# Kernel optimization log

Measured on AMD Instinct MI355X. Metric: run time of the kernel, lower is better.

Reference implementation:

```python
import jax, jax.numpy as jnp
import numpy as np

B, N, DIM, H = 8, 4096, 768, 12
HD = DIM // H
SCALE = HD ** -0.5


def setup_inputs() -> dict:
    key = jax.random.key(0)
    ks = jax.random.split(key, 6)
    x = jax.random.normal(ks[0], (B, N, DIM), dtype=jnp.float32)
    # torch nn.Linear weights: [out_features, in_features]
    Wqkv = jax.random.normal(ks[1], (3 * DIM, DIM), dtype=jnp.float32) * (DIM ** -0.5)
    Wp = jax.random.normal(ks[2], (DIM, DIM), dtype=jnp.float32) * (DIM ** -0.5)
    bp = jnp.zeros((DIM,), dtype=jnp.float32)
    w_q = jax.random.normal(ks[3], (H, HD), dtype=jnp.float32)
    w_k = jax.random.normal(ks[4], (H, HD), dtype=jnp.float32)
    return {"x": x, "Wqkv": Wqkv, "Wp": Wp, "bp": bp, "w_q": w_q, "w_k": w_k}


def reference(x, Wqkv, Wp, bp, w_q, w_k):
    b, n, c = x.shape
    qkv = x @ Wqkv.T                                   # [B,N,3C]
    # rearrange 'B N (qkv H C) -> qkv B H N C'
    qkv = qkv.reshape(b, n, 3, H, HD).transpose(2, 0, 3, 1, 4)
    q, k, v = qkv[0], qkv[1], qkv[2]                   # each [B,H,N,hd]

    alpha = jnp.einsum('bhnc,hc->bhn', q, w_q) * SCALE
    alpha = jax.nn.softmax(alpha, axis=-1)             # [B,H,N]
    global_q = jnp.einsum('bhn,bhnc->bhc', alpha, q)   # [B,H,hd]

    p = global_q[:, :, None, :] * k                    # [B,H,N,hd]
    beta = jnp.einsum('bhnc,hc->bhn', p, w_k) * SCALE
    beta = jax.nn.softmax(beta, axis=-1)
    global_k = jnp.einsum('bhn,bhnc->bhc', beta, k)    # [B,H,hd]

    u = global_k[:, :, None, :] * v                    # [B,H,N,hd]
    q_flat = q.transpose(0, 2, 1, 3).reshape(b, n, c)  # 'B H N C -> B N (H C)'
    u_flat = u.transpose(0, 2, 1, 3).reshape(b, n, c)
    return u_flat @ Wp.T + bp + q_flat
```

## Files before the change

### kernel.cpp

```cpp
#include <hip/hip_runtime.h>
#include <hip/hip_bf16.h>
#include <cstdint>
#include <cstddef>

#define B_ 8
#define N_ 4096
#define DIM_ 768
#define H_ 12
#define M_ (B_*N_)
#define SCALE_ 0.125f
#define NS2 16
#define KDIM 768
#define NKT 12
#define NITER 6

typedef __attribute__((ext_vector_type(8))) short s8v;
typedef __attribute__((ext_vector_type(4))) float f4v;

__device__ inline float bf2f(unsigned short u) {
    unsigned v = ((unsigned)u) << 16;
    return __builtin_bit_cast(float, v);
}
__device__ inline unsigned short f2bf(float f) {
    unsigned u = __builtin_bit_cast(unsigned, f);
    return (unsigned short)((u + 0x7FFFu + ((u >> 16) & 1u)) >> 16);
}
__device__ inline void gload16(const void* g, void* l) {
    __builtin_amdgcn_global_load_lds(
        (const __attribute__((address_space(1))) void*)g,
        (__attribute__((address_space(3))) void*)l, 16, 0, 0);
}

#define BARX() __builtin_amdgcn_s_barrier()
#define PRIO1() __builtin_amdgcn_s_setprio(1)
#define PRIO0() __builtin_amdgcn_s_setprio(0)
#define VM4() asm volatile("s_waitcnt vmcnt(4)" ::: "memory")
#define VM0() asm volatile("s_waitcnt vmcnt(0)" ::: "memory")

__global__ __launch_bounds__(512, 2)
void gemm8(const unsigned short* __restrict__ A, int ldaE,
           const unsigned short* __restrict__ Bmat,
           unsigned short* __restrict__ Cb,
           const float* __restrict__ w_q,
           float* __restrict__ pv1, float* __restrict__ pms1,
           int ntn)
{
    __shared__ __align__(16) char smem[131072];
    const int tid = threadIdx.x;
    const int l = tid & 63, w = tid >> 6;
    const int lr = l & 15, g = l >> 4;
    const int wm = w >> 2, wn = w & 3;

    const int nwg = gridDim.x, cpx = nwg >> 3;
    const int bid = blockIdx.x;
    const int lg = (bid & 7) * cpx + (bid >> 3);
    const int tm = lg / ntn, tn = lg % ntn;
    const int m0 = tm * 256, n0 = tn * 256;

    const long ldaB = (long)ldaE * 2;
    const long ldbB = (long)KDIM * 2;

    const int srA = w * 8 + (l >> 3);
    const int kbs = (l & 7) * 16;
    const int kbx = kbs ^ ((srA & 7) << 4);
    long offA[2], offB[2];
    offA[0] = (long)(srA) * ldaB + kbx;
    offA[1] = (long)(128 + srA) * ldaB + kbx;
    offB[0] = (long)(((srA >> 5)) * 64 + (srA & 31)) * ldbB + kbx;
    offB[1] = (long)((2 + (srA >> 5)) * 64 + (srA & 31)) * ldbB + kbx;

    const char* Abase = (const char*)(A + (size_t)m0 * ldaE);
    const char* Bbase = (const char*)(Bmat + (size_t)n0 * KDIM);

    const int aoff = (wm * 64 + lr) * 128;
    const int boff = (wn * 32 + lr) * 128;
    const int kx0 = (g * 16) ^ ((lr & 7) << 4);
    const int kx1 = (64 + g * 16) ^ ((lr & 7) << 4);

    f4v acc[8][4] = {};
    s8v af[4][2];
    s8v bfr[2][2][2];

#define STG_A(buf_, qm_, kt_) { \
    const char* s0_ = Abase + (long)(kt_) * 2 + (long)(qm_) * 64 * ldaB; \
    char* d0_ = smem + ((buf_) * 4 + (qm_)) * 16384 + w * 1024; \
    gload16(s0_ + offA[0], d0_); \
    gload16(s0_ + offA[1], d0_ + 8192); }

#define STG_B(buf_, qn_, kt_) { \
    const char* s0_ = Bbase + (long)(kt_) * 2 + (long)(qn_) * 32 * ldbB; \
    char* d0_ = smem + ((buf_) * 4 + 2 + (qn_)) * 16384 + w * 1024; \
    gload16(s0_ + offB[0], d0_); \
    gload16(s0_ + offB[1], d0_ + 8192); }

#define DS_A(buf_, qm_) { \
    const char* ba_ = smem + ((buf_) * 4 + (qm_)) * 16384 + aoff; \
    af[0][0] = *(const s8v*)(ba_ +    0 + kx0); af[0][1] = *(const s8v*)(ba_ +    0 + kx1); \
    af[1][0] = *(const s8v*)(ba_ + 2048 + kx0); af[1][1] = *(const s8v*)(ba_ + 2048 + kx1); \
    af[2][0] = *(const s8v*)(ba_ + 4096 + kx0); af[2][1] = *(const s8v*)(ba_ + 4096 + kx1); \
    af[3][0] = *(const s8v*)(ba_ + 6144 + kx0); af[3][1] = *(const s8v*)(ba_ + 6144 + kx1); }

#define DS_B(buf_, qn_) { \
    const char* bb_ = smem + ((buf_) * 4 + 2 + (qn_)) * 16384 + boff; \
    bfr[qn_][0][0] = *(const s8v*)(bb_ +    0 + kx0); bfr[qn_][0][1] = *(const s8v*)(bb_ +    0 + kx1); \
    bfr[qn_][1][0] = *(const s8v*)(bb_ + 2048 + kx0); bfr[qn_][1][1] = *(const s8v*)(bb_ + 2048 + kx1); }

#define MM(fmg_, fng_, qn_, kk_) \
    acc[fmg_][fng_] = __builtin_amdgcn_mfma_f32_16x16x32_bf16(af[(fmg_)&3][kk_], bfr[qn_][(fng_)&1][kk_], acc[fmg_][fng_], 0, 0, 0);

#define MFMA8(qm_, qn_, kk_) \
    MM((qm_)*4+0, (qn_)*2+0, qn_, kk_) MM((qm_)*4+0, (qn_)*2+1, qn_, kk_) \
    MM((qm_)*4+1, (qn_)*2+0, qn_, kk_) MM((qm_)*4+1, (qn_)*2+1, qn_, kk_) \
    MM((qm_)*4+2, (qn_)*2+0, qn_, kk_) MM((qm_)*4+2, (qn_)*2+1, qn_, kk_) \
    MM((qm_)*4+3, (qn_)*2+0, qn_, kk_) MM((qm_)*4+3, (qn_)*2+1, qn_, kk_)

#define MFMA16(qm_, qn_) { MFMA8(qm_, qn_, 0) MFMA8(qm_, qn_, 1) }

    STG_A(0, 0, 0); STG_B(0, 0, 0); STG_A(0, 1, 0); STG_B(0, 1, 0);
    STG_A(1, 0, 64); STG_B(1, 0, 64);
    VM4(); BARX();

    for (int i = 0; i < NITER; ++i) {
        const int t1k = (2 * i + 1) * 64, t2k = (2 * i + 2) * 64, t3k = (2 * i + 3) * 64;
        const bool h2 = (2 * i + 2) < NKT, h3 = (2 * i + 3) < NKT;
        const bool last = (i == NITER - 1);
        DS_A(0, 0); DS_B(0, 0); STG_B(1, 1, t1k);
        BARX(); PRIO1(); MFMA16(0, 0); PRIO0(); BARX();
        DS_B(0, 1); STG_A(1, 1, t1k);
        BARX(); PRIO1(); MFMA16(0, 1); PRIO0(); BARX();
        DS_A(0, 1); if (h2) STG_A(0, 0, t2k);
        BARX(); PRIO1(); MFMA16(1, 0); PRIO0(); BARX();
        if (h2) STG_B(0, 0, t2k);
        BARX(); PRIO1(); MFMA16(1, 1); PRIO0();
        if (last) { VM0(); } else { VM4(); }
        BARX();
        DS_A(1, 0); DS_B(1, 0); if (h2) STG_A(0, 1, t2k);
        BARX(); PRIO1(); MFMA16(0, 0); PRIO0(); BARX();
        DS_B(1, 1); if (h2) STG_B(0, 1, t2k);
        BARX(); PRIO1(); MFMA16(0, 1); PRIO0(); BARX();
        DS_A(1, 1); if (h3) STG_A(1, 0, t3k);
        BARX(); PRIO1(); MFMA16(1, 0); PRIO0(); BARX();
        if (h3) STG_B(1, 0, t3k);
        BARX(); PRIO1(); MFMA16(1, 1); PRIO0();
        if (last) { VM0(); } else { VM4(); }
        BARX();
    }

    if (tn >= 3) {
        const int c0 = (tn - 3) * 256;
#pragma unroll
        for (int fmg = 0; fmg < 8; ++fmg) {
#pragma unroll
            for (int fng = 0; fng < 4; ++fng) {
                const int col = c0 + wn * 64 + fng * 16 + lr;
#pragma unroll
                for (int r = 0; r < 4; ++r) {
                    const int row = m0 + wm * 128 + fmg * 16 + g * 4 + r;
                    Cb[(size_t)row * DIM_ + col] = f2bf(acc[fmg][fng][r]);
                }
            }
        }
    }

    if (tn < 3) {
        const int h = tn * 4 + wn;
        float wq[4];
#pragma unroll
        for (int f = 0; f < 4; ++f) wq[f] = w_q[h * 64 + f * 16 + lr];

        float d[8][4];
#pragma unroll
        for (int fmg = 0; fmg < 8; ++fmg) {
#pragma unroll
            for (int r = 0; r < 4; ++r) {
                float s = acc[fmg][0][r] * wq[0] + acc[fmg][1][r] * wq[1]
                        + acc[fmg][2][r] * wq[2] + acc[fmg][3][r] * wq[3];
                s += __shfl_xor(s, 1); s += __shfl_xor(s, 2);
                s += __shfl_xor(s, 4); s += __shfl_xor(s, 8);
                d[fmg][r] = s * SCALE_;
            }
        }
        float mw = d[0][0];
#pragma unroll
        for (int fmg = 0; fmg < 8; ++fmg)
#pragma unroll
            for (int r = 0; r < 4; ++r) mw = fmaxf(mw, d[fmg][r]);
        mw = fmaxf(mw, __shfl_xor(mw, 16));
        mw = fmaxf(mw, __shfl_xor(mw, 32));

        float ssum = 0.f;
        float pvec[4] = {};
#pragma unroll
        for (int fmg = 0; fmg < 8; ++fmg) {
#pragma unroll
            for (int r = 0; r < 4; ++r) {
                const float e = __expf(d[fmg][r] - mw);
                ssum += e;
#pragma unroll
                for (int f = 0; f < 4; ++f) pvec[f] += e * acc[fmg][f][r];
            }
        }
        ssum += __shfl_xor(ssum, 16); ssum += __shfl_xor(ssum, 32);
#pragma unroll
        for (int f = 0; f < 4; ++f) {
            pvec[f] += __shfl_xor(pvec[f], 16);
            pvec[f] += __shfl_xor(pvec[f], 32);
        }

        const int b = m0 >> 12;
        const int bh = b * H_ + h;
        const int slice = ((m0 & (N_ - 1)) >> 7) + wm;
        if (g == 0) {
#pragma unroll
            for (int f = 0; f < 4; ++f)
                pv1[(size_t)(bh * 32 + slice) * 64 + f * 16 + lr] = pvec[f];
            if (lr == 0) {
                pms1[(bh * 32 + slice) * 2] = mw;
                pms1[(bh * 32 + slice) * 2 + 1] = ssum;
            }
        }
    }
#undef STG_A
#undef STG_B
#undef DS_A
#undef DS_B
#undef MM
#undef MFMA8
#undef MFMA16
}

template<int MODE>
__global__ __launch_bounds__(512, 2)
void gemm128(const unsigned short* __restrict__ A, int ldaE,
             const unsigned short* __restrict__ Bmat,
             float* __restrict__ Cf, unsigned short* __restrict__ CbO,
             const float* __restrict__ bias, const float* __restrict__ addW,
             int Nc, int ntn)
{
    __shared__ __align__(16) char smem[98304];
    const int tid = threadIdx.x;
    const int l = tid & 63, w = tid >> 6;
    const int lr = l & 15, g = l >> 4;
    const int wm = w >> 2, wn = w & 3;

    const int nwg = gridDim.x, cpx = nwg >> 3;
    const int bid = blockIdx.x;
    const int lg = (bid & 7) * cpx + (bid >> 3);
    const int tm = lg / ntn, tn = lg % ntn;
    const int m0 = tm * 128, n0 = tn * 256;

    const long ldaB = (long)ldaE * 2;
    const long ldbB = (long)KDIM * 2;

    const unsigned short* Bp = Bmat;
    if (MODE == 0) Bp = Bmat + (size_t)(m0 >> 12) * (DIM_ * DIM_);

    const int srA = w * 8 + (l >> 3);
    const int kbs = (l & 7) * 16;
    const int kbx = kbs ^ ((srA & 7) << 4);
    long offA[2], offB[2];
    offA[0] = (long)(srA) * ldaB + kbx;
    offA[1] = (long)(64 + srA) * ldaB + kbx;
    offB[0] = (long)(((srA >> 5)) * 64 + (srA & 31)) * ldbB + kbx;
    offB[1] = (long)((2 + (srA >> 5)) * 64 + (srA & 31)) * ldbB + kbx;

    const char* Abase = (const char*)(A + (size_t)m0 * ldaE);
    const char* Bbase = (const char*)(Bp + (size_t)n0 * KDIM);

    const int aoff = (wm * 64 + lr) * 128;
    const int boff = (wn * 32 + lr) * 128;
    const int kx0 = (g * 16) ^ ((lr & 7) << 4);
    const int kx1 = (64 + g * 16) ^ ((lr & 7) << 4);

    f4v acc[4][4] = {};
    s8v af[4][2];
    s8v bfr[2][2][2];

#define STG_A1(buf_, kt_) { \
    const char* s0_ = Abase + (long)(kt_) * 2; \
    char* d0_ = smem + ((buf_) * 3) * 16384 + w * 1024; \
    gload16(s0_ + offA[0], d0_); \
    gload16(s0_ + offA[1], d0_ + 8192); }

#define STG_B1(buf_, qn_, kt_) { \
    const char* s0_ = Bbase + (long)(kt_) * 2 + (long)(qn_) * 32 * ldbB; \
    char* d0_ = smem + ((buf_) * 3 + 1 + (qn_)) * 16384 + w * 1024; \
    gload16(s0_ + offB[0], d0_); \
    gload16(s0_ + offB[1], d0_ + 8192); }

#define DS_A1(buf_) { \
    const char* ba_ = smem + ((buf_) * 3) * 16384 + aoff; \
    af[0][0] = *(const s8v*)(ba_ +    0 + kx0); af[0][1] = *(const s8v*)(ba_ +    0 + kx1); \
    af[1][0] = *(const s8v*)(ba_ + 2048 + kx0); af[1][1] = *(const s8v*)(ba_ + 2048 + kx1); \
    af[2][0] = *(const s8v*)(ba_ + 4096 + kx0); af[2][1] = *(const s8v*)(ba_ + 4096 + kx1); \
    af[3][0] = *(const s8v*)(ba_ + 6144 + kx0); af[3][1] = *(const s8v*)(ba_ + 6144 + kx1); }

#define DS_B1(buf_, qn_) { \
    const char* bb_ = smem + ((buf_) * 3 + 1 + (qn_)) * 16384 + boff; \
    bfr[qn_][0][0] = *(const s8v*)(bb_ +    0 + kx0); bfr[qn_][0][1] = *(const s8v*)(bb_ +    0 + kx1); \
    bfr[qn_][1][0] = *(const s8v*)(bb_ + 2048 + kx0); bfr[qn_][1][1] = *(const s8v*)(bb_ + 2048 + kx1); }

#define MM1(fm_, fng_, qn_, kk_) \
    acc[fm_][fng_] = __builtin_amdgcn_mfma_f32_16x16x32_bf16(af[fm_][kk_], bfr[qn_][(fng_)&1][kk_], acc[fm_][fng_], 0, 0, 0);

#define MFMA16_1(qn_, kk_) \
    MM1(0, (qn_)*2+0, qn_, kk_) MM1(0, (qn_)*2+1, qn_, kk_) \
    MM1(1, (qn_)*2+0, qn_, kk_) MM1(1, (qn_)*2+1, qn_, kk_) \
    MM1(2, (qn_)*2+0, qn_, kk_) MM1(2, (qn_)*2+1, qn_, kk_) \
    MM1(3, (qn_)*2+0, qn_, kk_) MM1(3, (qn_)*2+1, qn_, kk_)

#define MFMA32_1(qn_) { MFMA16_1(qn_, 0) MFMA16_1(qn_, 1) }

    STG_A1(0, 0); STG_B1(0, 0, 0); STG_B1(0, 1, 0);
    STG_A1(1, 64); STG_B1(1, 0, 64);
    VM4(); BARX();

    for (int i = 0; i < NITER; ++i) {
        const int t1k = (2 * i + 1) * 64, t2k = (2 * i + 2) * 64, t3k = (2 * i + 3) * 64;
        const bool h2 = (2 * i + 2) < NKT, h3 = (2 * i + 3) < NKT;
        const bool last = (i == NITER - 1);
        DS_A1(0); DS_B1(0, 0); STG_B1(1, 1, t1k);
        BARX(); PRIO1(); MFMA32_1(0); PRIO0(); BARX();
        DS_B1(0, 1); if (h2) { STG_A1(0, t2k); STG_B1(0, 0, t2k); }
        BARX(); PRIO1(); MFMA32_1(1); PRIO0();
        if (last) { VM0(); } else { VM4(); }
        BARX();
        DS_A1(1); DS_B1(1, 0); if (h2) STG_B1(0, 1, t2k);
        BARX(); PRIO1(); MFMA32_1(0); PRIO0(); BARX();
        DS_B1(1, 1); if (h3) { STG_A1(1, t3k); STG_B1(1, 0, t3k); }
        BARX(); PRIO1(); MFMA32_1(1); PRIO0();
        if (last) { VM0(); } else { VM4(); }
        BARX();
    }

    const int jb = m0 % DIM_;
#pragma unroll
    for (int fm = 0; fm < 4; ++fm) {
#pragma unroll
        for (int fng = 0; fng < 4; ++fng) {
            const int col = n0 + wn * 64 + fng * 16 + lr;
#pragma unroll
            for (int r = 0; r < 4; ++r) {
                const int ro = wm * 64 + fm * 16 + g * 4 + r;
                const int row = m0 + ro;
                if (MODE == 0) {
                    Cf[(size_t)row * Nc + col] = acc[fm][fng][r] + bias[col];
                } else {
                    CbO[(size_t)row * Nc + col] =
                        f2bf(acc[fm][fng][r] + addW[(size_t)(jb + ro) * DIM_ + col]);
                }
            }
        }
    }
#undef STG_A1
#undef STG_B1
#undef DS_A1
#undef DS_B1
#undef MM1
#undef MFMA16_1
#undef MFMA32_1
}

__global__ __launch_bounds__(256)
void fused_b(const unsigned short* __restrict__ kb,
             const float* __restrict__ pv1, const float* __restrict__ pms1,
             const float* __restrict__ w_k,
             float* __restrict__ pv2, float* __restrict__ pms2)
{
    const int bid = blockIdx.x;
    const int bh = bid / NS2, sp = bid % NS2;
    const int b = bh / H_, h = bh % H_;
    const int t = threadIdx.x;
    const int lane8 = t & 7, grp = t >> 3;

    __shared__ float gq_s[64];
    if (t < 64) {
        float mstar = pms1[(bh * 32) * 2];
#pragma unroll
        for (int p = 1; p < 32; ++p) mstar = fmaxf(mstar, pms1[(bh * 32 + p) * 2]);
        float sstar = 0.f, v = 0.f;
#pragma unroll
        for (int p = 0; p < 32; ++p) {
            const float e = __expf(pms1[(bh * 32 + p) * 2] - mstar);
            sstar += pms1[(bh * 32 + p) * 2 + 1] * e;
            v += pv1[(size_t)(bh * 32 + p) * 64 + t] * e;
        }
        gq_s[t] = (v / sstar) * w_k[h * 64 + t];
    }
    __syncthreads();

    float w8[8];
#pragma unroll
    for (int j = 0; j < 8; j++) w8[j] = gq_s[lane8 * 8 + j];

    const unsigned short* base = kb + ((size_t)(b * N_ + sp * 256) * DIM_)
                                 + h * 64 + lane8 * 8;
    float q[8][8];
    float d[8];
#pragma unroll
    for (int pass = 0; pass < 8; ++pass) {
        const int row = pass * 32 + grp;
        s8v q8 = *(const s8v*)(base + (size_t)row * DIM_);
        float s = 0.f;
#pragma unroll
        for (int j = 0; j < 8; j++) {
            q[pass][j] = bf2f((unsigned short)q8[j]);
            s += q[pass][j] * w8[j];
        }
        s += __shfl_xor(s, 1); s += __shfl_xor(s, 2); s += __shfl_xor(s, 4);
        d[pass] = s * SCALE_;
    }
    float m = d[0];
#pragma unroll
    for (int pass = 1; pass < 8; ++pass) m = fmaxf(m, d[pass]);
    float ssum = 0.f;
    float a8[8] = {};
#pragma unroll
    for (int pass = 0; pass < 8; ++pass) {
        float e = __expf(d[pass] - m);
        ssum += e;
#pragma unroll
        for (int j = 0; j < 8; j++) a8[j] += e * q[pass][j];
    }

    __shared__ float Lm[32], Ls[32];
    __shared__ float La[32][64];
    if (lane8 == 0) { Lm[grp] = m; Ls[grp] = ssum; }
#pragma unroll
    for (int j = 0; j < 8; j++) La[grp][lane8 * 8 + j] = a8[j];
    __syncthreads();

    if (t < 64) {
        float mstar = Lm[0];
#pragma unroll
        for (int g2 = 1; g2 < 32; ++g2) mstar = fmaxf(mstar, Lm[g2]);
        float sstar = 0.f, v = 0.f;
#pragma unroll
        for (int g2 = 0; g2 < 32; ++g2) {
            float e = __expf(Lm[g2] - mstar);
            sstar += Ls[g2] * e;
            v += La[g2][t] * e;
        }
        pv2[(size_t)bid * 64 + t] = v;
        if (t == 0) { pms2[bid * 2] = mstar; pms2[bid * 2 + 1] = sstar; }
    }
}

__global__ void path_reduce(const float* __restrict__ partv, const float* __restrict__ partms,
                            int nsp, float* __restrict__ gout)
{
    const int bh = blockIdx.x;
    const int t = threadIdx.x;
    float mstar = partms[(bh * nsp) * 2];
    for (int p = 1; p < nsp; ++p) mstar = fmaxf(mstar, partms[(bh * nsp + p) * 2]);
    float sstar = 0.f, v = 0.f;
    for (int p = 0; p < nsp; ++p) {
        float e = __expf(partms[(bh * nsp + p) * 2] - mstar);
        sstar += partms[(bh * nsp + p) * 2 + 1] * e;
        v += partv[(size_t)(bh * nsp + p) * 64 + t] * e;
    }
    gout[bh * 64 + t] = v / sstar;
}

__global__ void cvt_all(const float* __restrict__ x, const float* __restrict__ Wqkv,
                        unsigned short* __restrict__ xb, unsigned short* __restrict__ wqkb,
                        unsigned short* __restrict__ wvT,
                        int n4x, int n4xw)
{
    int i = blockIdx.x * 256 + threadIdx.x;
    if (i < n4xw) {
        const float* src; unsigned short* dst; int k;
        if (i < n4x) { src = x; dst = xb; k = i; }
        else { src = Wqkv; dst = wqkb; k = i - n4x; }
        float4 v = ((const float4*)src)[k];
        ushort4 o;
        o.x = f2bf(v.x); o.y = f2bf(v.y); o.z = f2bf(v.z); o.w = f2bf(v.w);
        ((ushort4*)dst)[k] = o;
    } else {
        const int k = i - n4xw;
        const int ii = k % DIM_;
        const int c0 = (k / DIM_) * 4;
        ushort4 o;
        o.x = f2bf(Wqkv[(size_t)(2 * DIM_ + c0 + 0) * DIM_ + ii]);
        o.y = f2bf(Wqkv[(size_t)(2 * DIM_ + c0 + 1) * DIM_ + ii]);
        o.z = f2bf(Wqkv[(size_t)(2 * DIM_ + c0 + 2) * DIM_ + ii]);
        o.w = f2bf(Wqkv[(size_t)(2 * DIM_ + c0 + 3) * DIM_ + ii]);
        *(ushort4*)&wvT[(size_t)ii * DIM_ + c0] = o;
    }
}

__global__ __launch_bounds__(256)
void fold_wp(const float* __restrict__ Wp, const float* __restrict__ gk,
             unsigned short* __restrict__ W2)
{
    int idx = blockIdx.x * 256 + threadIdx.x;
    int e4 = idx * 4;
    int b = (int)((unsigned)e4 / (unsigned)(DIM_ * DIM_));
    int rem = e4 - b * (DIM_ * DIM_);
    int c = rem % DIM_;
    float4 wv = *(const float4*)&Wp[rem];
    const float* gp = &gk[b * DIM_ + c];
    ushort4 o;
    o.x = f2bf(wv.x * gp[0]); o.y = f2bf(wv.y * gp[1]);
    o.z = f2bf(wv.z * gp[2]); o.w = f2bf(wv.w * gp[3]);
    *(ushort4*)&W2[e4] = o;
}

extern "C" void kernel_launch(void* const* d_in, const int* in_sizes, int n_in,
                              void* d_out, int out_size, void* d_ws, size_t ws_size,
                              hipStream_t stream)
{
    const float* x    = (const float*)d_in[0];
    const float* Wqkv = (const float*)d_in[1];
    const float* Wp   = (const float*)d_in[2];
    const float* bp   = (const float*)d_in[3];
    const float* w_q  = (const float*)d_in[4];
    const float* w_k  = (const float*)d_in[5];
    float* out = (float*)d_out;

    constexpr size_t NXB  = (size_t)M_ * DIM_;
    constexpr size_t NWQK = (size_t)2 * DIM_ * DIM_;
    constexpr size_t NWV  = (size_t)DIM_ * DIM_;
    constexpr size_t NKB  = (size_t)M_ * DIM_;
    constexpr size_t NW2  = (size_t)B_ * DIM_ * DIM_;

    char* p = (char*)d_ws;
    unsigned short* xb    = (unsigned short*)p; p += NXB * 2;
    unsigned short* wqkb  = (unsigned short*)p; p += NWQK * 2;
    unsigned short* wvT   = (unsigned short*)p; p += NWV * 2;
    unsigned short* kb    = (unsigned short*)p; p += NKB * 2;
    unsigned short* w2b   = (unsigned short*)p; p += NW2 * 2;
    unsigned short* w4b   = (unsigned short*)p; p += NW2 * 2;
    float* pv1  = (float*)p; p += (size_t)B_ * H_ * 32 * 64 * 4;
    float* pms1 = (float*)p; p += (size_t)B_ * H_ * 32 * 2 * 4;
    float* pv2  = (float*)p; p += (size_t)B_ * H_ * NS2 * 64 * 4;
    float* pms2 = (float*)p; p += (size_t)B_ * H_ * NS2 * 2 * 4;
    float* gkv  = (float*)p; p += (size_t)B_ * H_ * 64 * 4;

    constexpr int N4X  = (int)(NXB / 4);
    constexpr int N4XW = N4X + (int)(NWQK / 4);
    constexpr int NTOT = N4XW + (int)(NWV / 4);
    cvt_all<<<NTOT / 256, 256, 0, stream>>>(x, Wqkv, xb, wqkb, wvT, N4X, N4XW);

    gemm8<<<128 * 6, 512, 0, stream>>>(xb, DIM_, wqkb, kb, w_q, pv1, pms1, 6);

    fused_b<<<B_ * H_ * NS2, 256, 0, stream>>>(kb, pv1, pms1, w_k, pv2, pms2);

    path_reduce<<<B_ * H_, 64, 0, stream>>>(pv2, pms2, NS2, gkv);

    fold_wp<<<(int)(NW2 / 4 / 256), 256, 0, stream>>>(Wp, gkv, w2b);

    gemm128<1><<<48 * 3, 512, 0, stream>>>(w2b, DIM_, wvT, nullptr, w4b, nullptr, Wqkv,
                                           DIM_, 3);

    gemm128<0><<<256 * 3, 512, 0, stream>>>(xb, DIM_, w4b, out, nullptr, bp, nullptr,
                                            DIM_, 3);
}
```

Before: 207.1 us.

## Fold w_q into Wq to skip the Q projection GEMM, pool x instead

Instead of computing the full Q projection (x·Wqᵀ) and then dotting it with w_q, the kernel precomputes per-head vectors a_h = Wq_hᵀ·w_q, so the alpha logits become x·a_h. A new tile path in gemm8 computes these logits and the softmax partial stats, then accumulates alpha-weighted sums of raw x rows per slice. A new reduce_a kernel multiplies the pooled x by Wq to get global_q. This removes one third of the large QKV GEMM's output tiles (grid 768 to 512 blocks). In exchange it adds avec_prep, a 768-wide pooled-x partial per slice, and a final small GEMV per (b,h). Logits are now computed from bf16 a_h, which changes rounding.

```diff
diff --git a/kernel.cpp b/kernel.cpp
--- a/kernel.cpp
+++ b/kernel.cpp
@@ -41,7 +41,7 @@
 void gemm8(const unsigned short* __restrict__ A, int ldaE,
            const unsigned short* __restrict__ Bmat,
            unsigned short* __restrict__ Cb,
-           const float* __restrict__ w_q,
+           const unsigned short* __restrict__ avecb,
            float* __restrict__ pv1, float* __restrict__ pms1,
            int ntn)
 {
@@ -77,10 +77,6 @@
     const int kx0 = (g * 16) ^ ((lr & 7) << 4);
     const int kx1 = (64 + g * 16) ^ ((lr & 7) << 4);
 
-    f4v acc[8][4] = {};
-    s8v af[4][2];
-    s8v bfr[2][2][2];
-
 #define STG_A(buf_, qm_, kt_) { \
     const char* s0_ = Abase + (long)(kt_) * 2 + (long)(qm_) * 64 * ldaB; \
     char* d0_ = smem + ((buf_) * 4 + (qm_)) * 16384 + w * 1024; \
@@ -92,6 +88,11 @@
     char* d0_ = smem + ((buf_) * 4 + 2 + (qn_)) * 16384 + w * 1024; \
     gload16(s0_ + offB[0], d0_); \
     gload16(s0_ + offB[1], d0_ + 8192); }
+
+    if (tn < 3) {
+        f4v acc[8][4] = {};
+        s8v af[4][2];
+        s8v bfr[2][2][2];
 
 #define DS_A(buf_, qm_) { \
     const char* ba_ = smem + ((buf_) * 4 + (qm_)) * 16384 + aoff; \
@@ -116,38 +117,37 @@
 
 #define MFMA16(qm_, qn_) { MFMA8(qm_, qn_, 0) MFMA8(qm_, qn_, 1) }
 
-    STG_A(0, 0, 0); STG_B(0, 0, 0); STG_A(0, 1, 0); STG_B(0, 1, 0);
-    STG_A(1, 0, 64); STG_B(1, 0, 64);
-    VM4(); BARX();
-
-    for (int i = 0; i < NITER; ++i) {
-        const int t1k = (2 * i + 1) * 64, t2k = (2 * i + 2) * 64, t3k = (2 * i + 3) * 64;
-        const bool h2 = (2 * i + 2) < NKT, h3 = (2 * i + 3) < NKT;
-        const bool last = (i == NITER - 1);
-        DS_A(0, 0); DS_B(0, 0); STG_B(1, 1, t1k);
-        BARX(); PRIO1(); MFMA16(0, 0); PRIO0(); BARX();
-        DS_B(0, 1); STG_A(1, 1, t1k);
-        BARX(); PRIO1(); MFMA16(0, 1); PRIO0(); BARX();
-        DS_A(0, 1); if (h2) STG_A(0, 0, t2k);
-        BARX(); PRIO1(); MFMA16(1, 0); PRIO0(); BARX();
-        if (h2) STG_B(0, 0, t2k);
-        BARX(); PRIO1(); MFMA16(1, 1); PRIO0();
-        if (last) { VM0(); } else { VM4(); }
-        BARX();
-        DS_A(1, 0); DS_B(1, 0); if (h2) STG_A(0, 1, t2k);
-        BARX(); PRIO1(); MFMA16(0, 0); PRIO0(); BARX();
-        DS_B(1, 1); if (h2) STG_B(0, 1, t2k);
-        BARX(); PRIO1(); MFMA16(0, 1); PRIO0(); BARX();
-        DS_A(1, 1); if (h3) STG_A(1, 0, t3k);
-        BARX(); PRIO1(); MFMA16(1, 0); PRIO0(); BARX();
-        if (h3) STG_B(1, 0, t3k);
-        BARX(); PRIO1(); MFMA16(1, 1); PRIO0();
-        if (last) { VM0(); } else { VM4(); }
-        BARX();
-    }
-
-    if (tn >= 3) {
-        const int c0 = (tn - 3) * 256;
+        STG_A(0, 0, 0); STG_B(0, 0, 0); STG_A(0, 1, 0); STG_B(0, 1, 0);
+        STG_A(1, 0, 64); STG_B(1, 0, 64);
+        VM4(); BARX();
+
+        for (int i = 0; i < NITER; ++i) {
+            const int t1k = (2 * i + 1) * 64, t2k = (2 * i + 2) * 64, t3k = (2 * i + 3) * 64;
+            const bool h2 = (2 * i + 2) < NKT, h3 = (2 * i + 3) < NKT;
+            const bool last = (i == NITER - 1);
+            DS_A(0, 0); DS_B(0, 0); STG_B(1, 1, t1k);
+            BARX(); PRIO1(); MFMA16(0, 0); PRIO0(); BARX();
+            DS_B(0, 1); STG_A(1, 1, t1k);
+            BARX(); PRIO1(); MFMA16(0, 1); PRIO0(); BARX();
+            DS_A(0, 1); if (h2) STG_A(0, 0, t2k);
+            BARX(); PRIO1(); MFMA16(1, 0); PRIO0(); BARX();
+            if (h2) STG_B(0, 0, t2k);
+            BARX(); PRIO1(); MFMA16(1, 1); PRIO0();
+            if (last) { VM0(); } else { VM4(); }
+            BARX();
+            DS_A(1, 0); DS_B(1, 0); if (h2) STG_A(0, 1, t2k);
+            BARX(); PRIO1(); MFMA16(0, 0); PRIO0(); BARX();
+            DS_B(1, 1); if (h2) STG_B(0, 1, t2k);
+            BARX(); PRIO1(); MFMA16(0, 1); PRIO0(); BARX();
+            DS_A(1, 1); if (h3) STG_A(1, 0, t3k);
+            BARX(); PRIO1(); MFMA16(1, 0); PRIO0(); BARX();
+            if (h3) STG_B(1, 0, t3k);
+            BARX(); PRIO1(); MFMA16(1, 1); PRIO0();
+            if (last) { VM0(); } else { VM4(); }
+            BARX();
+        }
+
+        const int c0 = tn * 256;
 #pragma unroll
         for (int fmg = 0; fmg < 8; ++fmg) {
 #pragma unroll
@@ -160,73 +160,136 @@
                 }
             }
         }
-    }
-
-    if (tn < 3) {
-        const int h = tn * 4 + wn;
-        float wq[4];
-#pragma unroll
-        for (int f = 0; f < 4; ++f) wq[f] = w_q[h * 64 + f * 16 + lr];
-
-        float d[8][4];
-#pragma unroll
-        for (int fmg = 0; fmg < 8; ++fmg) {
-#pragma unroll
-            for (int r = 0; r < 4; ++r) {
-                float s = acc[fmg][0][r] * wq[0] + acc[fmg][1][r] * wq[1]
-                        + acc[fmg][2][r] * wq[2] + acc[fmg][3][r] * wq[3];
-                s += __shfl_xor(s, 1); s += __shfl_xor(s, 2);
-                s += __shfl_xor(s, 4); s += __shfl_xor(s, 8);
-                d[fmg][r] = s * SCALE_;
-            }
-        }
-        float mw = d[0][0];
-#pragma unroll
-        for (int fmg = 0; fmg < 8; ++fmg)
-#pragma unroll
-            for (int r = 0; r < 4; ++r) mw = fmaxf(mw, d[fmg][r]);
-        mw = fmaxf(mw, __shfl_xor(mw, 16));
-        mw = fmaxf(mw, __shfl_xor(mw, 32));
-
-        float ssum = 0.f;
-        float pvec[4] = {};
-#pragma unroll
-        for (int fmg = 0; fmg < 8; ++fmg) {
-#pragma unroll
-            for (int r = 0; r < 4; ++r) {
-                const float e = __expf(d[fmg][r] - mw);
-                ssum += e;
-#pragma unroll
-                for (int f = 0; f < 4; ++f) pvec[f] += e * acc[fmg][f][r];
-            }
-        }
-        ssum += __shfl_xor(ssum, 16); ssum += __shfl_xor(ssum, 32);
-#pragma unroll
-        for (int f = 0; f < 4; ++f) {
-            pvec[f] += __shfl_xor(pvec[f], 16);
-            pvec[f] += __shfl_xor(pvec[f], 32);
-        }
-
-        const int b = m0 >> 12;
-        const int bh = b * H_ + h;
-        const int slice = ((m0 & (N_ - 1)) >> 7) + wm;
-        if (g == 0) {
-#pragma unroll
-            for (int f = 0; f < 4; ++f)
-                pv1[(size_t)(bh * 32 + slice) * 64 + f * 16 + lr] = pvec[f];
-            if (lr == 0) {
-                pms1[(bh * 32 + slice) * 2] = mw;
-                pms1[(bh * 32 + slice) * 2 + 1] = ssum;
-            }
-        }
-    }
-#undef STG_A
-#undef STG_B
 #undef DS_A
 #undef DS_B
 #undef MM
 #undef MFMA8
 #undef MFMA16
+    } else {
+        const int b = m0 >> 12;
+        const int slice = (m0 & (N_ - 1)) >> 8;
+        if (w < 2) {
+            const int rw = l >> 3;
+            const int by = ((l & 7) * 16) ^ (rw << 4);
+#pragma unroll
+            for (int k6 = 0; k6 < 6; ++k6) {
+                const int kt = w * 6 + k6;
+                gload16((const char*)avecb + (size_t)rw * 1536 + kt * 128 + by,
+                        smem + 32768 + kt * 2048);
+                gload16((const char*)avecb + (size_t)(8 + rw) * 1536 + kt * 128 + by,
+                        smem + 32768 + kt * 2048 + 1024);
+            }
+        }
+        STG_A(0, 0, 0); STG_A(0, 1, 0);
+        STG_A(1, 0, 64); STG_A(1, 1, 64);
+        VM4(); BARX();
+
+        f4v sacc[2] = {};
+        for (int kt = 0; kt < 12; ++kt) {
+            const int buf = kt & 1;
+#pragma unroll
+            for (int j = 0; j < 2; ++j) {
+                const int r0 = w * 32 + j * 16;
+                const int qm = (r0 >> 6) & 1, hi = r0 >> 7, loc = r0 & 63;
+                const char* ab = smem + (buf * 4 + qm) * 16384 + hi * 8192 + (loc + lr) * 128;
+                s8v a0 = *(const s8v*)(ab + kx0);
+                s8v a1 = *(const s8v*)(ab + kx1);
+                const char* vb = smem + 32768 + kt * 2048 + lr * 128;
+                s8v b0 = *(const s8v*)(vb + kx0);
+                s8v b1 = *(const s8v*)(vb + kx1);
+                sacc[j] = __builtin_amdgcn_mfma_f32_16x16x32_bf16(a0, b0, sacc[j], 0, 0, 0);
+                sacc[j] = __builtin_amdgcn_mfma_f32_16x16x32_bf16(a1, b1, sacc[j], 0, 0, 0);
+            }
+            BARX();
+            if (kt + 2 < 12) {
+                const int kk2 = (kt + 2) * 64;
+                STG_A(buf, 0, kk2); STG_A(buf, 1, kk2);
+            }
+            if (kt <= 9) { VM4(); } else { VM0(); }
+            BARX();
+        }
+
+        float dd[8];
+#pragma unroll
+        for (int j = 0; j < 2; ++j)
+#pragma unroll
+            for (int r = 0; r < 4; ++r) dd[j * 4 + r] = sacc[j][r] * SCALE_;
+
+        float mw = dd[0];
+#pragma unroll
+        for (int q2 = 1; q2 < 8; ++q2) mw = fmaxf(mw, dd[q2]);
+        mw = fmaxf(mw, __shfl_xor(mw, 16));
+        mw = fmaxf(mw, __shfl_xor(mw, 32));
+        float* Lm = (float*)(smem + 107008);
+        float* Ls = (float*)(smem + 107520);
+        if (l < 16) Lm[w * 16 + lr] = mw;
+        __syncthreads();
+        float mfin = Lm[lr];
+#pragma unroll
+        for (int w2 = 1; w2 < 8; ++w2) mfin = fmaxf(mfin, Lm[w2 * 16 + lr]);
+
+        float ss = 0.f;
+#pragma unroll
+        for (int j = 0; j < 2; ++j)
+#pragma unroll
+            for (int r = 0; r < 4; ++r) {
+                const float e = __expf(dd[j * 4 + r] - mfin);
+                ss += e;
+                const int row = w * 32 + j * 16 + g * 4 + r;
+                *(unsigned short*)(smem + 98304 + lr * 544 + row * 2) = f2bf(e);
+            }
+        ss += __shfl_xor(ss, 16);
+        ss += __shfl_xor(ss, 32);
+        if (l < 16) Ls[w * 16 + lr] = ss;
+        __syncthreads();
+
+        if (tid < 12) {
+            float S = 0.f;
+#pragma unroll
+            for (int w2 = 0; w2 < 8; ++w2) S += Ls[w2 * 16 + tid];
+            float M2 = Lm[tid];
+#pragma unroll
+            for (int w2 = 1; w2 < 8; ++w2) M2 = fmaxf(M2, Lm[w2 * 16 + tid]);
+            pms1[((size_t)(b * H_ + tid) * 16 + slice) * 2 + 0] = M2;
+            pms1[((size_t)(b * H_ + tid) * 16 + slice) * 2 + 1] = S;
+        }
+        __syncthreads();
+
+        for (int it = 0; it < 6; ++it) {
+            const int ktA = it * 2, ktB = it * 2 + 1;
+            STG_A(0, 0, ktA * 64); STG_A(0, 1, ktA * 64);
+            STG_A(1, 0, ktB * 64); STG_A(1, 1, ktB * 64);
+            VM0(); BARX();
+            const int buf = w >> 2;
+            const int kt = it * 2 + buf;
+            const int d0 = (w & 3) * 16;
+            const int dby = (d0 + (l & 15)) * 2;
+            f4v pacc = {};
+#pragma unroll
+            for (int c = 0; c < 8; ++c) {
+                s8v ae = *(const s8v*)(smem + 98304 + (l & 15) * 544
+                                       + (c * 32 + (l >> 4) * 8) * 2);
+                const char* xr = smem + (buf * 4 + ((c >> 1) & 1)) * 16384 + (c >> 2) * 8192;
+                const int nb = (c & 1) * 32 + (l >> 4) * 8;
+                s8v bx;
+#pragma unroll
+                for (int j = 0; j < 8; ++j)
+                    bx[j] = (short)*(const unsigned short*)(xr + (nb + j) * 128 + (dby ^ (j << 4)));
+                pacc = __builtin_amdgcn_mfma_f32_16x16x32_bf16(ae, bx, pacc, 0, 0, 0);
+            }
+            if ((l >> 4) < 3) {
+#pragma unroll
+                for (int r = 0; r < 4; ++r) {
+                    const int h = (l >> 4) * 4 + r;
+                    pv1[((size_t)(b * 16 + slice) * 12 + h) * 768
+                        + kt * 64 + d0 + (l & 15)] = pacc[r];
+                }
+            }
+            BARX();
+        }
+    }
+#undef STG_A
+#undef STG_B
 }
 
 template<int MODE>
@@ -362,9 +425,46 @@
 }
 
 __global__ __launch_bounds__(256)
+void reduce_a(const float* __restrict__ pv1, const float* __restrict__ pms1,
+              const float* __restrict__ Wqkv, const float* __restrict__ w_k,
+              float* __restrict__ gqwk)
+{
+    const int b = blockIdx.x / H_, h = blockIdx.x % H_;
+    const int t = threadIdx.x;
+    __shared__ float Svec[768];
+    __shared__ float ew[16];
+    __shared__ float Ssh;
+
+    const float* pp = pms1 + (size_t)(b * H_ + h) * 16 * 2;
+    float M = pp[0];
+    for (int s = 1; s < 16; ++s) M = fmaxf(M, pp[s * 2]);
+    if (t < 16) ew[t] = __expf(pp[t * 2] - M);
+    __syncthreads();
+    if (t == 0) {
+        float S = 0.f;
+        for (int s = 0; s < 16; ++s) S += ew[s] * pp[s * 2 + 1];
+        Ssh = S;
+    }
+#pragma unroll
+    for (int j = 0; j < 3; ++j) {
+        const int col = t + j * 256;
+        float v = 0.f;
+        for (int s = 0; s < 16; ++s)
+            v += ew[s] * pv1[((size_t)(b * 16 + s) * 12 + h) * 768 + col];
+        Svec[col] = v;
+    }
+    __syncthreads();
+    if (t < 64) {
+        const float* wr = Wqkv + (size_t)(h * 64 + t) * 768;
+        float gg = 0.f;
+        for (int c = 0; c < 768; ++c) gg += wr[c] * Svec[c];
+        gqwk[(size_t)(b * H_ + h) * 64 + t] = (gg / Ssh) * w_k[h * 64 + t];
+    }
+}
+
+__global__ __launch_bounds__(256)
 void fused_b(const unsigned short* __restrict__ kb,
-             const float* __restrict__ pv1, const float* __restrict__ pms1,
-             const float* __restrict__ w_k,
+             const float* __restrict__ gqwk,
              float* __restrict__ pv2, float* __restrict__ pms2)
 {
     const int bid = blockIdx.x;
@@ -374,19 +474,7 @@
     const int lane8 = t & 7, grp = t >> 3;
 
     __shared__ float gq_s[64];
-    if (t < 64) {
-        float mstar = pms1[(bh * 32) * 2];
-#pragma unroll
-        for (int p = 1; p < 32; ++p) mstar = fmaxf(mstar, pms1[(bh * 32 + p) * 2]);
-        float sstar = 0.f, v = 0.f;
-#pragma unroll
-        for (int p = 0; p < 32; ++p) {
-            const float e = __expf(pms1[(bh * 32 + p) * 2] - mstar);
-            sstar += pms1[(bh * 32 + p) * 2 + 1] * e;
-            v += pv1[(size_t)(bh * 32 + p) * 64 + t] * e;
-        }
-        gq_s[t] = (v / sstar) * w_k[h * 64 + t];
-    }
+    if (t < 64) gq_s[t] = gqwk[(size_t)bh * 64 + t];
     __syncthreads();
 
     float w8[8];
@@ -462,6 +550,30 @@
     gout[bh * 64 + t] = v / sstar;
 }
 
+__global__ __launch_bounds__(256)
+void avec_prep(const float* __restrict__ Wqkv, const float* __restrict__ w_q,
+               unsigned short* __restrict__ avecb)
+{
+    const int h = blockIdx.x;
+    const int t = threadIdx.x;
+    if (h >= H_) {
+#pragma unroll
+        for (int j = 0; j < 3; ++j) avecb[(size_t)h * 768 + t + j * 256] = 0;
+        return;
+    }
+    __shared__ float wl[64];
+    if (t < 64) wl[t] = w_q[h * 64 + t];
+    __syncthreads();
+#pragma unroll
+    for (int j = 0; j < 3; ++j) {
+        const int dcol = t + j * 256;
+        float a = 0.f;
+        for (int c = 0; c < 64; ++c)
+            a += wl[c] * Wqkv[(size_t)(h * 64 + c) * 768 + dcol];
+        avecb[(size_t)h * 768 + dcol] = f2bf(a);
+    }
+}
+
 __global__ void cvt_all(const float* __restrict__ x, const float* __restrict__ Wqkv,
                         unsigned short* __restrict__ xb, unsigned short* __restrict__ wqkb,
                         unsigned short* __restrict__ wvT,
@@ -471,7 +583,7 @@
     if (i < n4xw) {
         const float* src; unsigned short* dst; int k;
         if (i < n4x) { src = x; dst = xb; k = i; }
-        else { src = Wqkv; dst = wqkb; k = i - n4x; }
+        else { src = Wqkv + (size_t)DIM_ * DIM_; dst = wqkb; k = i - n4x; }
         float4 v = ((const float4*)src)[k];
         ushort4 o;
         o.x = f2bf(v.x); o.y = f2bf(v.y); o.z = f2bf(v.z); o.w = f2bf(v.w);
@@ -518,34 +630,39 @@
     const float* w_k  = (const float*)d_in[5];
     float* out = (float*)d_out;
 
-    constexpr size_t NXB  = (size_t)M_ * DIM_;
-    constexpr size_t NWQK = (size_t)2 * DIM_ * DIM_;
-    constexpr size_t NWV  = (size_t)DIM_ * DIM_;
-    constexpr size_t NKB  = (size_t)M_ * DIM_;
-    constexpr size_t NW2  = (size_t)B_ * DIM_ * DIM_;
+    constexpr size_t NXB = (size_t)M_ * DIM_;
+    constexpr size_t NWK = (size_t)DIM_ * DIM_;
+    constexpr size_t NWV = (size_t)DIM_ * DIM_;
+    constexpr size_t NKB = (size_t)M_ * DIM_;
+    constexpr size_t NW2 = (size_t)B_ * DIM_ * DIM_;
 
     char* p = (char*)d_ws;
     unsigned short* xb    = (unsigned short*)p; p += NXB * 2;
-    unsigned short* wqkb  = (unsigned short*)p; p += NWQK * 2;
+    unsigned short* wqkb  = (unsigned short*)p; p += NWK * 2;
     unsigned short* wvT   = (unsigned short*)p; p += NWV * 2;
     unsigned short* kb    = (unsigned short*)p; p += NKB * 2;
     unsigned short* w2b   = (unsigned short*)p; p += NW2 * 2;
     unsigned short* w4b   = (unsigned short*)p; p += NW2 * 2;
-    float* pv1  = (float*)p; p += (size_t)B_ * H_ * 32 * 64 * 4;
-    float* pms1 = (float*)p; p += (size_t)B_ * H_ * 32 * 2 * 4;
+    unsigned short* avecb = (unsigned short*)p; p += (size_t)16 * 768 * 2;
+    float* pv1  = (float*)p; p += (size_t)B_ * 16 * 12 * 768 * 4;
+    float* pms1 = (float*)p; p += (size_t)B_ * H_ * 16 * 2 * 4;
     float* pv2  = (float*)p; p += (size_t)B_ * H_ * NS2 * 64 * 4;
     float* pms2 = (float*)p; p += (size_t)B_ * H_ * NS2 * 2 * 4;
+    float* gqwk = (float*)p; p += (size_t)B_ * H_ * 64 * 4;
     float* gkv  = (float*)p; p += (size_t)B_ * H_ * 64 * 4;
 
     constexpr int N4X  = (int)(NXB / 4);
-    constexpr int N4XW = N4X + (int)(NWQK / 4);
+    constexpr int N4XW = N4X + (int)(NWK / 4);
     constexpr int NTOT = N4XW + (int)(NWV / 4);
     cvt_all<<<NTOT / 256, 256, 0, stream>>>(x, Wqkv, xb, wqkb, wvT, N4X, N4XW);
 
-    gemm8<<<128 * 6, 512, 0, stream>>>(xb, DIM_, wqkb, kb, w_q, pv1, pms1, 6);
-
-    fused_b<<<B_ * H_ * NS2, 256, 0, stream>>>(kb, pv1, pms1, w_k, pv2, pms2);
-
+    avec_prep<<<16, 256, 0, stream>>>(Wqkv, w_q, avecb);
+
+    gemm8<<<128 * 4, 512, 0, stream>>>(xb, DIM_, wqkb, kb, avecb, pv1, pms1, 4);
+
+    reduce_a<<<B_ * H_, 256, 0, stream>>>(pv1, pms1, Wqkv, w_k, gqwk);
+
+    fused_b<<<B_ * H_ * NS2, 256, 0, stream>>>(kb, gqwk, pv2, pms2);
     path_reduce<<<B_ * H_, 64, 0, stream>>>(pv2, pms2, NS2, gkv);
 
     fold_wp<<<(int)(NW2 / 4 / 256), 256, 0, stream>>>(Wp, gkv, w2b);
```

Result: slower. 214.7 us (+3.7%).
